# Kernel tuning notes

Measured on AMD Instinct MI355X. Metric: run time of the kernel, lower is better.

The kernel has to match this reference:

```python
import jax, jax.numpy as jnp
import numpy as np

N_NODES = 50000
N_EDGES = 1_600_000
F_IN = 64
HID = 128
HEADS = 8
D_HEAD = HID // HEADS
N_LAYERS = 2
LEAKY_SLOPE = 0.2
LN_EPS = 1e-5


def setup_inputs() -> dict:
    key = jax.random.key(0)
    ks = jax.random.split(key, 10)
    s = 0.05
    return {
        "node_features": jax.random.normal(ks[0], (N_NODES, F_IN), jnp.float32),
        "edge_index": jax.random.randint(ks[1], (2, N_EDGES), 0, N_NODES, jnp.int64),
        "W_in": jax.random.normal(ks[2], (F_IN, HID), jnp.float32) * s,
        "b_in": jnp.zeros((HID,), jnp.float32),
        "W": jax.random.normal(ks[3], (N_LAYERS, HID, HID), jnp.float32) * s,
        "a_src": jax.random.normal(ks[4], (N_LAYERS, HEADS, D_HEAD), jnp.float32) * s,
        "a_dst": jax.random.normal(ks[5], (N_LAYERS, HEADS, D_HEAD), jnp.float32) * s,
        "b_gat": jnp.zeros((N_LAYERS, HID), jnp.float32),
        "ln_g": jnp.ones((N_LAYERS, HID), jnp.float32),
        "ln_b": jnp.zeros((N_LAYERS, HID), jnp.float32),
    }


def _layer_norm(x, g, b):
    mu = jnp.mean(x, axis=-1, keepdims=True)
    var = jnp.mean(jnp.square(x - mu), axis=-1, keepdims=True)
    return (x - mu) * jax.lax.rsqrt(var + LN_EPS) * g + b


def _gat_forward(node_features, edge_index, W_in, b_in, W, a_src, a_dst, b_gat, ln_g, ln_b):
    src = edge_index[0]
    dst = edge_index[1]
    # input projection (dropout is identity in eval mode)
    x = node_features @ W_in + b_in  # [N, HID]
    for i in range(N_LAYERS):
        residual = x
        h = (x @ W[i]).reshape(N_NODES, HEADS, D_HEAD)  # [N, H, d]
        alpha_s = jnp.einsum('nhd,hd->nh', h, a_src[i])  # [N, H]
        alpha_d = jnp.einsum('nhd,hd->nh', h, a_dst[i])  # [N, H]
        e = alpha_s[src] + alpha_d[dst]                  # [E, H]
        e = jnp.where(e > 0, e, LEAKY_SLOPE * e)         # LeakyReLU(0.2)
        # softmax over incoming edges of each destination node
        e_max = jax.ops.segment_max(e, dst, num_segments=N_NODES)  # [N, H]
        ex = jnp.exp(e - e_max[dst])
        denom = jax.ops.segment_sum(ex, dst, num_segments=N_NODES)  # [N, H]
        att = ex / denom[dst]                            # [E, H]
        msg = att[:, :, None] * h[src]                   # [E, H, d]
        out = jax.ops.segment_sum(msg, dst, num_segments=N_NODES)  # [N, H, d]
        out = out.reshape(N_NODES, HID) + b_gat[i]
        out = jax.nn.elu(out)                            # GAT activation (concat heads)
        x = _layer_norm(out + residual, ln_g[i], ln_b[i])
    return x


def reference(node_features, edge_index, W_in, b_in, W, a_src, a_dst, b_gat, ln_g, ln_b):
    return _gat_forward(node_features, edge_index, W_in, b_in, W, a_src, a_dst, b_gat, ln_g, ln_b)
```

## Files before the change

### kernel.cpp

```cpp
#include <hip/hip_runtime.h>
#include <hip/hip_bf16.h>
#include <math.h>


#define F_IN 64
#define HID 128
#define HEADS 8

#define RBITS 8
#define RNODES 256
#define NB 196
#define REPL 8
#define CAP_R 1920
#define PADI 16
#define BCAPB (REPL * CAP_R)
#define TILE 4096

typedef unsigned short ushort_t;
typedef unsigned char  uchar_t;
typedef float vf2 __attribute__((ext_vector_type(2)));

static __device__ __forceinline__ int xcd_id() {
    int x;
    asm volatile("s_getreg_b32 %0, hwreg(20, 0, 32)" : "=s"(x));
    return x & (REPL - 1);
}


static __device__ __forceinline__ unsigned fp8_enc1(float f) {
    unsigned u = __float_as_uint(f);
    unsigned s = (u >> 24) & 0x80u;
    u &= 0x7fffffffu;
    float af = __uint_as_float(u);
    unsigned r;
    if (af >= 448.f) {
        r = 0x7eu;
    } else if (af >= 0.015625f) {
        unsigned t = u + 0x7ffffu + ((u >> 20) & 1u);
        r = (t >> 20) - 960u;
        if (r > 0x7eu) r = 0x7eu;
    } else {
        r = (unsigned)(int)(af * 512.f + 0.5f);
    }
    return r | s;
}

static __device__ __forceinline__ unsigned f32x4_to_fp8(float a, float b, float c, float d) {
#if __has_builtin(__builtin_amdgcn_cvt_pk_fp8_f32)
    int v = 0;
    v = __builtin_amdgcn_cvt_pk_fp8_f32(a, b, v, false);
    v = __builtin_amdgcn_cvt_pk_fp8_f32(c, d, v, true);
    return (unsigned)v;
#else
    return fp8_enc1(a) | (fp8_enc1(b) << 8) | (fp8_enc1(c) << 16) | (fp8_enc1(d) << 24);
#endif
}

static __device__ __forceinline__ void fp8x4_to_f32(unsigned w, float* f) {
#if __has_builtin(__builtin_amdgcn_cvt_pk_f32_fp8)
    vf2 lo = __builtin_amdgcn_cvt_pk_f32_fp8((int)w, false);
    vf2 hi = __builtin_amdgcn_cvt_pk_f32_fp8((int)w, true);
    f[0] = lo[0]; f[1] = lo[1]; f[2] = hi[0]; f[3] = hi[1];
#else
    #pragma unroll
    for (int i = 0; i < 4; i++) {
        unsigned b = (w >> (8 * i)) & 0xffu;
        float v = __uint_as_float(((b & 0x80u) << 24) | ((b & 0x7fu) << 20));
        f[i] = v * 0x1p120f;
    }
#endif
}


__global__ __launch_bounds__(256) void partition_kernel(
        const int* __restrict__ ei, int E,
        int* __restrict__ bcur, unsigned int* __restrict__ part) {
    __shared__ unsigned ed[TILE];
    __shared__ int cnt[256], st[256], cur[256], gbase[256];
    int t = threadIdx.x;
    int lane = t & 63;
    int is64 = __any(ei[2 * lane + 1] != 0) ? 0 : 1;
    int r = xcd_id();
    int base = blockIdx.x * TILE;

    cnt[t] = 0;
    __syncthreads();

    unsigned pk[16];
    #pragma unroll
    for (int k = 0; k < 16; k++) {
        int idx = base + k * 256 + t;
        unsigned p;
        if (idx < E) {
            int s, d;
            if (is64) { s = ei[2 * (size_t)idx]; d = ei[2 * (size_t)E + 2 * (size_t)idx]; }
            else      { s = ei[idx];             d = ei[(size_t)E + idx]; }
            p = (unsigned)s | ((unsigned)(d & 255) << 16) | ((unsigned)(d >> 8) << 24);
        } else {
            p = 0xffffffffu;
        }
        pk[k] = p;
        atomicAdd(&cnt[p >> 24], 1);
    }
    __syncthreads();

    if (t < 64) {
        int c0 = cnt[4 * t], c1 = cnt[4 * t + 1], c2 = cnt[4 * t + 2], c3 = cnt[4 * t + 3];
        int s = c0 + c1 + c2 + c3;
        int inc = s;
        #pragma unroll
        for (int off = 1; off < 64; off <<= 1) {
            int o = __shfl_up(inc, off);
            if (lane >= off) inc += o;
        }
        int ex = inc - s;
        st[4 * t] = ex; st[4 * t + 1] = ex + c0;
        st[4 * t + 2] = ex + c0 + c1; st[4 * t + 3] = ex + c0 + c1 + c2;
    }
    __syncthreads();
    cur[t] = st[t];
    __syncthreads();

    #pragma unroll
    for (int k = 0; k < 16; k++) {
        unsigned p = pk[k];
        int pos = atomicAdd(&cur[p >> 24], 1);
        ed[pos] = p;
    }
    __syncthreads();

    if (t < NB) {
        int c = cnt[t];
        gbase[t] = (c > 0)
            ? (int)atomicAdd((unsigned*)&bcur[(t * REPL + r) * PADI], (unsigned)c) : 0;
    }
    __syncthreads();

    for (int i = t; i < TILE; i += 256) {
        unsigned p = ed[i];
        int b = p >> 24;
        if (b >= NB) continue;
        int g = gbase[b] + (i - st[b]);
        if (g < CAP_R)
            part[(size_t)(b * REPL + r) * CAP_R + g] = p & 0xffffffu;
    }
}

__global__ __launch_bounds__(256) void bsort_kernel(
        const unsigned int* __restrict__ part, const int* __restrict__ bcur,
        uint2* __restrict__ nodeinfo, ushort_t* __restrict__ src_sorted, int N) {
    __shared__ unsigned ed[BCAPB];
    __shared__ int cnt[256], sc[256], cur[256];
    int b = blockIdx.x, t = threadIdx.x;
    int lane = t & 63;
    int base = b * BCAPB;
    int ofs = 0;
    #pragma unroll
    for (int rr = 0; rr < REPL; rr++) {
        int c = min(bcur[(b * REPL + rr) * PADI], CAP_R);
        for (int i = t; i < c; i += 256) ed[ofs + i] = part[(size_t)(b * REPL + rr) * CAP_R + i];
        ofs += c;
    }
    int total = ofs;
    cnt[t] = 0;
    __syncthreads();
    for (int i = t; i < total; i += 256) atomicAdd(&cnt[(ed[i] >> 16) & 255], 1);
    __syncthreads();
    if (t < 64) {
        int c0 = cnt[4 * t], c1 = cnt[4 * t + 1], c2 = cnt[4 * t + 2], c3 = cnt[4 * t + 3];
        int s = c0 + c1 + c2 + c3;
        int inc = s;
        #pragma unroll
        for (int off = 1; off < 64; off <<= 1) {
            int o = __shfl_up(inc, off);
            if (lane >= off) inc += o;
        }
        int ex = inc - s;
        sc[4 * t] = ex; sc[4 * t + 1] = ex + c0;
        sc[4 * t + 2] = ex + c0 + c1; sc[4 * t + 3] = ex + c0 + c1 + c2;
    }
    __syncthreads();
    int node = b * RNODES + t;
    if (node < N) nodeinfo[node] = make_uint2((unsigned)(base + sc[t]), (unsigned)cnt[t]);
    cur[t] = sc[t];
    __syncthreads();
    for (int i = t; i < total; i += 256) {
        unsigned e = ed[i];
        int d = (e >> 16) & 255;
        int p = atomicAdd(&cur[d], 1);
        src_sorted[base + p] = (ushort_t)(e & 0xffffu);
    }
}

template<int K, bool IN_PROJ>
__global__ __launch_bounds__(256) void gemm_kernel(
        const float* __restrict__ A, const float* __restrict__ B,
        const float* __restrict__ bias,
        const float* __restrict__ asv, const float* __restrict__ adv,
        float* __restrict__ xout, uchar_t* __restrict__ hb8,
        float* __restrict__ alpha_s, float* __restrict__ alpha_d, int M) {
    __shared__ float Al[64 * 32];
    __shared__ float Bl[32 * 128];
    int t = threadIdx.x;
    int r0 = blockIdx.x * 64;
    int c4 = (t & 31) * 4;
    int rg = t >> 5;
    float4 acc[8];
    #pragma unroll
    for (int j = 0; j < 8; j++) acc[j] = make_float4(0.f, 0.f, 0.f, 0.f);

    for (int kc = 0; kc < K / 32; kc++) {
        __syncthreads();
        {
            int row = t >> 3, q = (t & 7) * 4;
            #pragma unroll
            for (int half = 0; half < 2; half++) {
                int rr = row + half * 32;
                int gr = r0 + rr;
                float4 v = make_float4(0.f, 0.f, 0.f, 0.f);
                if (gr < M) v = *(const float4*)(A + (size_t)gr * K + kc * 32 + q);
                *(float4*)&Al[rr * 32 + q] = v;
            }
        }
        {
            #pragma unroll
            for (int p = 0; p < 4; p++) {
                int idx = p * 256 + t;
                int br = idx >> 5, bq = (idx & 31) * 4;
                *(float4*)&Bl[br * 128 + bq] =
                    *(const float4*)(B + (size_t)(kc * 32 + br) * 128 + bq);
            }
        }
        __syncthreads();
        #pragma unroll
        for (int k = 0; k < 32; k += 4) {
            float4 b0 = *(float4*)&Bl[(k + 0) * 128 + c4];
            float4 b1 = *(float4*)&Bl[(k + 1) * 128 + c4];
            float4 b2 = *(float4*)&Bl[(k + 2) * 128 + c4];
            float4 b3 = *(float4*)&Bl[(k + 3) * 128 + c4];
            #pragma unroll
            for (int j = 0; j < 8; j++) {
                float4 a = *(float4*)&Al[(rg * 8 + j) * 32 + k];
                acc[j].x += a.x * b0.x; acc[j].y += a.x * b0.y;
                acc[j].z += a.x * b0.z; acc[j].w += a.x * b0.w;
                acc[j].x += a.y * b1.x; acc[j].y += a.y * b1.y;
                acc[j].z += a.y * b1.z; acc[j].w += a.y * b1.w;
                acc[j].x += a.z * b2.x; acc[j].y += a.z * b2.y;
                acc[j].z += a.z * b2.z; acc[j].w += a.z * b2.w;
                acc[j].x += a.w * b3.x; acc[j].y += a.w * b3.y;
                acc[j].z += a.w * b3.z; acc[j].w += a.w * b3.w;
            }
        }
    }

    if (IN_PROJ) {
        float4 bv = *(const float4*)(bias + c4);
        #pragma unroll
        for (int j = 0; j < 8; j++) {
            int r = r0 + rg * 8 + j;
            if (r >= M) continue;
            float4 o = acc[j];
            o.x += bv.x; o.y += bv.y; o.z += bv.z; o.w += bv.w;
            *(float4*)(xout + (size_t)r * 128 + c4) = o;
        }
    } else {
        float4 asf = *(const float4*)(asv + c4);
        float4 adf = *(const float4*)(adv + c4);
        int head = (t & 31) >> 2;
        #pragma unroll
        for (int j = 0; j < 8; j++) {
            int r = r0 + rg * 8 + j;
            if (r >= M) continue;
            float4 o = acc[j];
            unsigned pkv = f32x4_to_fp8(o.x, o.y, o.z, o.w);
            *(unsigned*)(hb8 + (size_t)r * 128 + c4) = pkv;
            float ps = o.x * asf.x + o.y * asf.y + o.z * asf.z + o.w * asf.w;
            float pd = o.x * adf.x + o.y * adf.y + o.z * adf.z + o.w * adf.w;
            ps += __shfl_xor(ps, 1); ps += __shfl_xor(ps, 2);
            pd += __shfl_xor(pd, 1); pd += __shfl_xor(pd, 2);
            if ((t & 3) == 0) {
                alpha_s[(size_t)r * HEADS + head] = ps;
                alpha_d[(size_t)r * HEADS + head] = pd;
            }
        }
    }
}


__global__ __launch_bounds__(256) void agg_kernel(
        const uint2* __restrict__ nodeinfo, const ushort_t* __restrict__ src_sorted,
        const uchar_t* __restrict__ hb8,
        const float* __restrict__ al_s,
        const float* __restrict__ al_d,
        const float* __restrict__ x_res, float* __restrict__ x_out,
        const float* __restrict__ bg, const float* __restrict__ g,
        const float* __restrict__ bb, int N) {
    int wid = threadIdx.x >> 6, lane = threadIdx.x & 63;
    int n = blockIdx.x * 4 + wid;
    if (n >= N) return;
    uint2 nd = nodeinfo[n];
    int beg = (int)nd.x;
    int deg = (int)nd.y;
    int es = lane >> 4;
    int q  = lane & 15;
    int head = q >> 1;
    float ad = al_d[(size_t)n * 8 + head];

    float acc[8] = {0.f, 0.f, 0.f, 0.f, 0.f, 0.f, 0.f, 0.f};
    float den = 0.f;

    for (int p = 0; p < deg; p += 8) {
        int e0 = p + es, e1 = p + 4 + es;
        bool v0 = e0 < deg, v1 = e1 < deg;
        int s0 = v0 ? (int)src_sorted[beg + e0] : 0;
        int s1 = v1 ? (int)src_sorted[beg + e1] : 0;
        float A0 = al_s[(size_t)s0 * 8 + head];
        float A1 = al_s[(size_t)s1 * 8 + head];
        uint2 h0 = *(const uint2*)(hb8 + (size_t)s0 * 128 + q * 8);
        uint2 h1 = *(const uint2*)(hb8 + (size_t)s1 * 128 + q * 8);
        float ev0 = A0 + ad; ev0 = ev0 > 0.f ? ev0 : 0.2f * ev0;
        float ev1 = A1 + ad; ev1 = ev1 > 0.f ? ev1 : 0.2f * ev1;
        float w0 = v0 ? __expf(ev0) : 0.f;
        float w1 = v1 ? __expf(ev1) : 0.f;
        den += w0 + w1;
        float f0[8], f1[8];
        fp8x4_to_f32(h0.x, f0); fp8x4_to_f32(h0.y, f0 + 4);
        fp8x4_to_f32(h1.x, f1); fp8x4_to_f32(h1.y, f1 + 4);
        #pragma unroll
        for (int j = 0; j < 8; j++) acc[j] += w0 * f0[j] + w1 * f1[j];
    }

    #pragma unroll
    for (int j = 0; j < 8; j++) {
        acc[j] += __shfl_xor(acc[j], 16);
        acc[j] += __shfl_xor(acc[j], 32);
    }
    den += __shfl_xor(den, 16);
    den += __shfl_xor(den, 32);

    float inv = (deg > 0) ? 1.f / den : 0.f;

    float4 bga = *(const float4*)(bg + q * 8);
    float4 bgb = *(const float4*)(bg + q * 8 + 4);
    float4 rva = *(const float4*)(x_res + (size_t)n * 128 + q * 8);
    float4 rvb = *(const float4*)(x_res + (size_t)n * 128 + q * 8 + 4);
    float v[8];
    v[0] = acc[0] * inv + bga.x; v[1] = acc[1] * inv + bga.y;
    v[2] = acc[2] * inv + bga.z; v[3] = acc[3] * inv + bga.w;
    v[4] = acc[4] * inv + bgb.x; v[5] = acc[5] * inv + bgb.y;
    v[6] = acc[6] * inv + bgb.z; v[7] = acc[7] * inv + bgb.w;
    #pragma unroll
    for (int j = 0; j < 8; j++) v[j] = v[j] > 0.f ? v[j] : __expf(v[j]) - 1.f;
    v[0] += rva.x; v[1] += rva.y; v[2] += rva.z; v[3] += rva.w;
    v[4] += rvb.x; v[5] += rvb.y; v[6] += rvb.z; v[7] += rvb.w;

    float sloc = ((v[0] + v[1]) + (v[2] + v[3])) + ((v[4] + v[5]) + (v[6] + v[7]));
    sloc += __shfl_xor(sloc, 1); sloc += __shfl_xor(sloc, 2);
    sloc += __shfl_xor(sloc, 4); sloc += __shfl_xor(sloc, 8);
    float mu = sloc * (1.f / 128.f);
    float vs = 0.f;
    #pragma unroll
    for (int j = 0; j < 8; j++) { float d = v[j] - mu; vs += d * d; }
    vs += __shfl_xor(vs, 1); vs += __shfl_xor(vs, 2);
    vs += __shfl_xor(vs, 4); vs += __shfl_xor(vs, 8);
    float rstd = rsqrtf(vs * (1.f / 128.f) + 1e-5f);

    if (es == 0) {
        float4 ga = *(const float4*)(g + q * 8);
        float4 gb = *(const float4*)(g + q * 8 + 4);
        float4 ba = *(const float4*)(bb + q * 8);
        float4 b2 = *(const float4*)(bb + q * 8 + 4);
        float4 oa, ob;
        oa.x = (v[0] - mu) * rstd * ga.x + ba.x;
        oa.y = (v[1] - mu) * rstd * ga.y + ba.y;
        oa.z = (v[2] - mu) * rstd * ga.z + ba.z;
        oa.w = (v[3] - mu) * rstd * ga.w + ba.w;
        ob.x = (v[4] - mu) * rstd * gb.x + b2.x;
        ob.y = (v[5] - mu) * rstd * gb.y + b2.y;
        ob.z = (v[6] - mu) * rstd * gb.z + b2.z;
        ob.w = (v[7] - mu) * rstd * gb.w + b2.w;
        *(float4*)(x_out + (size_t)n * 128 + q * 8) = oa;
        *(float4*)(x_out + (size_t)n * 128 + q * 8 + 4) = ob;
    }
}


extern "C" void kernel_launch(void* const* d_in, const int* in_sizes, int n_in,
                              void* d_out, int out_size, void* d_ws, size_t ws_size,
                              hipStream_t stream) {
    const float* nf    = (const float*)d_in[0];
    const int*   ei    = (const int*)d_in[1];
    const float* W_in  = (const float*)d_in[2];
    const float* b_in  = (const float*)d_in[3];
    const float* W     = (const float*)d_in[4];
    const float* a_src = (const float*)d_in[5];
    const float* a_dst = (const float*)d_in[6];
    const float* b_gat = (const float*)d_in[7];
    const float* ln_g  = (const float*)d_in[8];
    const float* ln_b  = (const float*)d_in[9];
    float* out = (float*)d_out;

    const int N = in_sizes[0] / F_IN;
    const int E = in_sizes[1] / 2;
    const int NBKT = (N + RNODES - 1) >> RBITS;

    size_t off = 0;
    auto alloc = [&](size_t bytes) -> void* {
        void* p = (char*)d_ws + off;
        off += (bytes + 255) & ~(size_t)255;
        return p;
    };
    uint2*    nodeinfo   = (uint2*)alloc(sizeof(uint2) * N);
    int*      bcur       = (int*)alloc(sizeof(int) * (size_t)NBKT * REPL * PADI);
    unsigned* part       = (unsigned*)alloc(sizeof(unsigned) * (size_t)NBKT * REPL * CAP_R);
    ushort_t* src_sorted = (ushort_t*)alloc(sizeof(ushort_t) * (size_t)NBKT * BCAPB);
    float*    x          = (float*)alloc(sizeof(float) * (size_t)N * HID);
    uchar_t*  hb8        = (uchar_t*)alloc(sizeof(uchar_t) * (size_t)N * HID);
    float*    al_s       = (float*)alloc(sizeof(float) * (size_t)N * HEADS);
    float*    al_d       = (float*)alloc(sizeof(float) * (size_t)N * HEADS);
    (void)ws_size;

    hipMemsetAsync(bcur, 0, sizeof(int) * (size_t)NBKT * REPL * PADI, stream);
    int ptiles = (E + TILE - 1) / TILE;
    partition_kernel<<<ptiles, 256, 0, stream>>>(ei, E, bcur, part);
    bsort_kernel<<<NBKT, 256, 0, stream>>>(part, bcur, nodeinfo, src_sorted, N);

    int gemm_grid = (N + 63) / 64;
    gemm_kernel<F_IN, true><<<gemm_grid, 256, 0, stream>>>(
        nf, W_in, b_in, nullptr, nullptr, x, nullptr, nullptr, nullptr, N);

    int ngb = (N + 3) / 4;
    for (int layer = 0; layer < 2; layer++) {
        gemm_kernel<HID, false><<<gemm_grid, 256, 0, stream>>>(
            x, W + (size_t)layer * HID * HID, nullptr,
            a_src + (size_t)layer * HID, a_dst + (size_t)layer * HID,
            nullptr, hb8, al_s, al_d, N);
        float* xo = (layer == 1) ? out : x;
        agg_kernel<<<ngb, 256, 0, stream>>>(
            nodeinfo, src_sorted, hb8, al_s, al_d,
            x, xo,
            b_gat + (size_t)layer * HID, ln_g + (size_t)layer * HID,
            ln_b + (size_t)layer * HID, N);
    }
}
```

Baseline: 244.8 us.

## Replace scalar FP32 GEMMs with bf16 MFMA tiles and pre-transposed bf16 weights

Replaces the FP32 FMA register-tiled GEMM with 16x16x32 bf16 MFMA instructions. A new prep kernel converts and transposes the weights to bf16, and activations are converted to bf16 while being staged in shared memory. Results go back through shared memory so the existing epilogues stay unchanged. This cuts the ALU cost of the three dense projections, at the price of bf16 rounding on inputs and one extra small kernel launch.

```diff
diff --git a/kernel.cpp b/kernel.cpp
--- a/kernel.cpp
+++ b/kernel.cpp
@@ -19,11 +19,19 @@
 typedef unsigned short ushort_t;
 typedef unsigned char  uchar_t;
 typedef float vf2 __attribute__((ext_vector_type(2)));
+typedef short bf16x8 __attribute__((ext_vector_type(8)));
+typedef float f32x4 __attribute__((ext_vector_type(4)));
 
 static __device__ __forceinline__ int xcd_id() {
     int x;
     asm volatile("s_getreg_b32 %0, hwreg(20, 0, 32)" : "=s"(x));
     return x & (REPL - 1);
+}
+
+static __device__ __forceinline__ ushort_t f2bf(float f) {
+    unsigned int u = __float_as_uint(f);
+    unsigned int r = (u + 0x7fffu + ((u >> 16) & 1u)) >> 16;
+    return (ushort_t)r;
 }
 
 
@@ -192,74 +200,86 @@
     }
 }
 
+
+__global__ __launch_bounds__(256) void prep_kernel(
+        const float* __restrict__ Win, const float* __restrict__ W,
+        ushort_t* __restrict__ wt_in, ushort_t* __restrict__ wt0,
+        ushort_t* __restrict__ wt1) {
+    int t0 = blockIdx.x * 256 + threadIdx.x;
+    int stride = gridDim.x * 256;
+    for (int i = t0; i < 128 * 64; i += stride) {
+        int n = i >> 6, k = i & 63;
+        wt_in[i] = f2bf(Win[k * 128 + n]);
+    }
+    for (int i = t0; i < 128 * 128; i += stride) {
+        int n = i >> 7, k = i & 127;
+        wt0[i] = f2bf(W[k * 128 + n]);
+        wt1[i] = f2bf(W[128 * 128 + k * 128 + n]);
+    }
+}
+
+
 template<int K, bool IN_PROJ>
 __global__ __launch_bounds__(256) void gemm_kernel(
-        const float* __restrict__ A, const float* __restrict__ B,
+        const float* __restrict__ A, const ushort_t* __restrict__ Wt,
         const float* __restrict__ bias,
         const float* __restrict__ asv, const float* __restrict__ adv,
         float* __restrict__ xout, uchar_t* __restrict__ hb8,
         float* __restrict__ alpha_s, float* __restrict__ alpha_d, int M) {
-    __shared__ float Al[64 * 32];
-    __shared__ float Bl[32 * 128];
+    constexpr int KP = K + 8;
+    __shared__ union {
+        struct { ushort_t a[64 * KP]; ushort_t b[128 * KP]; } s;
+        float c[64 * 132];
+    } u;
     int t = threadIdx.x;
+    int w = t >> 6, l = t & 63;
     int r0 = blockIdx.x * 64;
+
+    for (int idx = t; idx < 64 * (K / 4); idx += 256) {
+        int row = idx / (K / 4), cc = (idx % (K / 4)) * 4;
+        int gr = r0 + row;
+        float4 v = (gr < M) ? *(const float4*)(A + (size_t)gr * K + cc)
+                            : make_float4(0.f, 0.f, 0.f, 0.f);
+        ushort4 h;
+        h.x = f2bf(v.x); h.y = f2bf(v.y); h.z = f2bf(v.z); h.w = f2bf(v.w);
+        *(ushort4*)&u.s.a[row * KP + cc] = h;
+    }
+    for (int idx = t; idx < 128 * (K / 8); idx += 256) {
+        int row = idx / (K / 8), k8 = (idx % (K / 8)) * 8;
+        *(uint4*)&u.s.b[row * KP + k8] = *(const uint4*)(Wt + (size_t)row * K + k8);
+    }
+    __syncthreads();
+
+    f32x4 acc[8];
+    #pragma unroll
+    for (int j = 0; j < 8; j++) acc[j] = (f32x4){0.f, 0.f, 0.f, 0.f};
+    int m = l & 15, kg = l >> 4;
+    #pragma unroll
+    for (int kk = 0; kk < K / 32; kk++) {
+        bf16x8 af = *(bf16x8*)&u.s.a[(w * 16 + m) * KP + kk * 32 + kg * 8];
+        #pragma unroll
+        for (int nt = 0; nt < 8; nt++) {
+            bf16x8 bfv = *(bf16x8*)&u.s.b[(nt * 16 + m) * KP + kk * 32 + kg * 8];
+            acc[nt] = __builtin_amdgcn_mfma_f32_16x16x32_bf16(af, bfv, acc[nt], 0, 0, 0);
+        }
+    }
+    __syncthreads();
+    #pragma unroll
+    for (int nt = 0; nt < 8; nt++)
+        #pragma unroll
+        for (int r = 0; r < 4; r++)
+            u.c[(w * 16 + kg * 4 + r) * 132 + nt * 16 + m] = acc[nt][r];
+    __syncthreads();
+
     int c4 = (t & 31) * 4;
     int rg = t >> 5;
-    float4 acc[8];
-    #pragma unroll
-    for (int j = 0; j < 8; j++) acc[j] = make_float4(0.f, 0.f, 0.f, 0.f);
-
-    for (int kc = 0; kc < K / 32; kc++) {
-        __syncthreads();
-        {
-            int row = t >> 3, q = (t & 7) * 4;
-            #pragma unroll
-            for (int half = 0; half < 2; half++) {
-                int rr = row + half * 32;
-                int gr = r0 + rr;
-                float4 v = make_float4(0.f, 0.f, 0.f, 0.f);
-                if (gr < M) v = *(const float4*)(A + (size_t)gr * K + kc * 32 + q);
-                *(float4*)&Al[rr * 32 + q] = v;
-            }
-        }
-        {
-            #pragma unroll
-            for (int p = 0; p < 4; p++) {
-                int idx = p * 256 + t;
-                int br = idx >> 5, bq = (idx & 31) * 4;
-                *(float4*)&Bl[br * 128 + bq] =
-                    *(const float4*)(B + (size_t)(kc * 32 + br) * 128 + bq);
-            }
-        }
-        __syncthreads();
-        #pragma unroll
-        for (int k = 0; k < 32; k += 4) {
-            float4 b0 = *(float4*)&Bl[(k + 0) * 128 + c4];
-            float4 b1 = *(float4*)&Bl[(k + 1) * 128 + c4];
-            float4 b2 = *(float4*)&Bl[(k + 2) * 128 + c4];
-            float4 b3 = *(float4*)&Bl[(k + 3) * 128 + c4];
-            #pragma unroll
-            for (int j = 0; j < 8; j++) {
-                float4 a = *(float4*)&Al[(rg * 8 + j) * 32 + k];
-                acc[j].x += a.x * b0.x; acc[j].y += a.x * b0.y;
-                acc[j].z += a.x * b0.z; acc[j].w += a.x * b0.w;
-                acc[j].x += a.y * b1.x; acc[j].y += a.y * b1.y;
-                acc[j].z += a.y * b1.z; acc[j].w += a.y * b1.w;
-                acc[j].x += a.z * b2.x; acc[j].y += a.z * b2.y;
-                acc[j].z += a.z * b2.z; acc[j].w += a.z * b2.w;
-                acc[j].x += a.w * b3.x; acc[j].y += a.w * b3.y;
-                acc[j].z += a.w * b3.z; acc[j].w += a.w * b3.w;
-            }
-        }
-    }
-
     if (IN_PROJ) {
         float4 bv = *(const float4*)(bias + c4);
         #pragma unroll
         for (int j = 0; j < 8; j++) {
             int r = r0 + rg * 8 + j;
             if (r >= M) continue;
-            float4 o = acc[j];
+            float4 o = *(float4*)&u.c[(rg * 8 + j) * 132 + c4];
             o.x += bv.x; o.y += bv.y; o.z += bv.z; o.w += bv.w;
             *(float4*)(xout + (size_t)r * 128 + c4) = o;
         }
@@ -271,7 +291,7 @@
         for (int j = 0; j < 8; j++) {
             int r = r0 + rg * 8 + j;
             if (r >= M) continue;
-            float4 o = acc[j];
+            float4 o = *(float4*)&u.c[(rg * 8 + j) * 132 + c4];
             unsigned pkv = f32x4_to_fp8(o.x, o.y, o.z, o.w);
             *(unsigned*)(hb8 + (size_t)r * 128 + c4) = pkv;
             float ps = o.x * asf.x + o.y * asf.y + o.z * asf.z + o.w * asf.w;
@@ -418,6 +438,9 @@
     uchar_t*  hb8        = (uchar_t*)alloc(sizeof(uchar_t) * (size_t)N * HID);
     float*    al_s       = (float*)alloc(sizeof(float) * (size_t)N * HEADS);
     float*    al_d       = (float*)alloc(sizeof(float) * (size_t)N * HEADS);
+    ushort_t* wt_in      = (ushort_t*)alloc(sizeof(ushort_t) * 128 * 64);
+    ushort_t* wt0        = (ushort_t*)alloc(sizeof(ushort_t) * 128 * 128);
+    ushort_t* wt1        = (ushort_t*)alloc(sizeof(ushort_t) * 128 * 128);
     (void)ws_size;
 
     hipMemsetAsync(bcur, 0, sizeof(int) * (size_t)NBKT * REPL * PADI, stream);
@@ -425,14 +448,15 @@
     partition_kernel<<<ptiles, 256, 0, stream>>>(ei, E, bcur, part);
     bsort_kernel<<<NBKT, 256, 0, stream>>>(part, bcur, nodeinfo, src_sorted, N);
 
+    prep_kernel<<<64, 256, 0, stream>>>(W_in, W, wt_in, wt0, wt1);
     int gemm_grid = (N + 63) / 64;
     gemm_kernel<F_IN, true><<<gemm_grid, 256, 0, stream>>>(
-        nf, W_in, b_in, nullptr, nullptr, x, nullptr, nullptr, nullptr, N);
+        nf, wt_in, b_in, nullptr, nullptr, x, nullptr, nullptr, nullptr, N);
 
     int ngb = (N + 3) / 4;
     for (int layer = 0; layer < 2; layer++) {
         gemm_kernel<HID, false><<<gemm_grid, 256, 0, stream>>>(
-            x, W + (size_t)layer * HID * HID, nullptr,
+            x, (layer == 0) ? wt0 : wt1, nullptr,
             a_src + (size_t)layer * HID, a_dst + (size_t)layer * HID,
             nullptr, hb8, al_s, al_d, N);
         float* xo = (layer == 1) ? out : x;
```

New measurement: 222.2 us. -9.2%, faster.
